# Kernel tuning notes

Measured on AMD Instinct MI355X. Metric: run time of the kernel, lower is better.

## Reference

```python
import jax, jax.numpy as jnp
import numpy as np

N_VOX = 500000
P, S, K = 2048, 64, 8          # pixels(rays), samples per ray, voxel neighbors per sample
F_M, F_H = 64, 128             # voxel feature dim, mlp hidden dim
FREQ_PE = 4
DEPTH_MIN, DEPTH_MAX = 1.0, 80.0
RAY_SAMPLE_STEPS = 64.0
EPS = 1e-10
IN_FEAT = F_M + 3 * FREQ_PE * 2  # 88


def lrelu(x):
    return jnp.where(x >= 0, x, 0.1 * x)  # LeakyReLU(0.1)


def posenc(x, L=FREQ_PE):
    # NeRF positional encoding: sin/cos(2^i * x), i in [0, L)
    freqs = 2.0 ** jnp.arange(L, dtype=x.dtype)          # [L]
    ang = x[..., None] * freqs                            # [..., 3, L]
    enc = jnp.concatenate([jnp.sin(ang), jnp.cos(ang)], axis=-1)  # [..., 3, 2L]
    return enc.reshape(x.shape[:-1] + (x.shape[-1] * 2 * L,))


def setup_inputs() -> dict:
    key = jax.random.key(0)
    ks = jax.random.split(key, 16)

    def xavier(k, fan_in, fan_out):
        return jax.random.normal(k, (fan_in, fan_out), jnp.float32) / np.sqrt(fan_in)

    inp = {
        'map_xyz': jax.random.normal(ks[0], (N_VOX, 3), jnp.float32),
        'map_feat': jax.random.normal(ks[1], (N_VOX, F_M), jnp.float32) * 0.05,
        'ind_voxel': jax.random.randint(ks[2], (P, S, K), 0, N_VOX),
        'sample_xyz': jax.random.normal(ks[3], (P, S, 3), jnp.float32),
        'dist_to_cam': jax.random.uniform(ks[4], (P, S), jnp.float32) * RAY_SAMPLE_STEPS,
        'W0': xavier(ks[5], IN_FEAT, F_H), 'b0': jnp.full((F_H,), 0.01, jnp.float32),
        'W1': xavier(ks[6], F_H, F_H),     'b1': jnp.full((F_H,), 0.01, jnp.float32),
        'W2': xavier(ks[7], F_H, F_H),     'b2': jnp.full((F_H,), 0.01, jnp.float32),
        'Wa0': xavier(ks[8], F_H, F_H // 2), 'ba0': jnp.full((F_H // 2,), 0.01, jnp.float32),
        'Wa1': xavier(ks[9], F_H // 2, 1),   'ba1': jnp.full((1,), 0.01, jnp.float32),
        'Wr0': xavier(ks[10], F_H, F_H // 2), 'br0': jnp.full((F_H // 2,), 0.01, jnp.float32),
        'Wr1': xavier(ks[11], F_H // 2, 3),   'br1': jnp.full((3,), 0.01, jnp.float32),
    }
    return inp


def reference(map_xyz, map_feat, ind_voxel, sample_xyz, dist_to_cam,
              W0, b0, W1, b1, W2, b2, Wa0, ba0, Wa1, ba1, Wr0, br0, Wr1, br1):
    # ---- voxel -> sample messages (func_msg_voxel_to_sample) ----
    voxel_xyz = map_xyz[ind_voxel]                       # [P,S,K,3] gather
    feat = map_feat[ind_voxel]                           # [P,S,K,F_M] gather
    offset = sample_xyz[:, :, None, :] - voxel_xyz       # [P,S,K,3]
    h = jnp.concatenate([feat, posenc(offset)], axis=-1) # [P,S,K,88]
    h = lrelu(h @ W0 + b0)
    h = lrelu(h @ W1 + b1)
    h = lrelu(h @ W2 + b2)                               # [P,S,K,F_H]
    w = jnp.exp(-10.0 * jnp.linalg.norm(offset, axis=-1))  # [P,S,K]
    w = w / jnp.sum(w, axis=-1, keepdims=True)
    # ---- reduce over K neighbors (func_reduce_voxel_to_sample) ----
    feat_s = jnp.sum(h * w[..., None], axis=2)           # [P,S,F_H]
    a = lrelu(feat_s @ Wa0 + ba0)
    alpha = jax.nn.sigmoid(a @ Wa1 + ba1)                # [P,S,1]
    r = lrelu(feat_s @ Wr0 + br0)
    rgb = jax.nn.sigmoid(r @ Wr1 + br1)                  # [P,S,3]
    # ---- sample -> pixel volume rendering (func_reduce_sample_to_pixel) ----
    dist = DEPTH_MIN + DEPTH_MAX * dist_to_cam / RAY_SAMPLE_STEPS  # [P,S]
    ones = jnp.ones((P, 1, 1), alpha.dtype)
    trans = jnp.cumprod(jnp.concatenate([ones, 1.0 - alpha + EPS], axis=1), axis=1)[:, :-1, :]
    blend = alpha * trans                                # [P,S,1]
    pixel_rgb = jnp.sum(rgb * blend, axis=1)             # [P,3]
    pixel_d = jnp.sum(dist[..., None] * blend, axis=1)   # [P,1]
    acc = jnp.sum(blend, axis=1)                         # [P,1]
    return jnp.concatenate([pixel_rgb, pixel_d, acc], axis=-1)  # [P,5]
```

## Files before the change

kernel.cpp:

```cpp
#include <hip/hip_runtime.h>

typedef __bf16 bf16_t;
typedef __bf16 bf16x2 __attribute__((ext_vector_type(2)));
typedef __bf16 bf16x4 __attribute__((ext_vector_type(4)));
typedef __bf16 bf16x8 __attribute__((ext_vector_type(8)));
typedef float  f32x4  __attribute__((ext_vector_type(4)));

#define NPIX 2048
#define NS   64
#define NK   8
#define NSAMP (NPIX*NS)
#define NROWS (NSAMP*NK)
#define TROWS 64
#define NTILES (NROWS/TROWS)
#define GRID   512
#define NIT    16
#define XSTR 104
#define HSTR 136

#define PK_W0 0
#define PK_W1 1536
#define PK_W2 3584
#define PK_WA 5632
#define PK_WR 6656
#define PK_TOT 7680

#define WS_AR_BYTES 122880

__global__ void pack_weights(const float* __restrict__ W0, const float* __restrict__ W1,
                             const float* __restrict__ W2, const float* __restrict__ Wa0,
                             const float* __restrict__ Wr0, bf16_t* __restrict__ dst0) {
  int tid = blockIdx.x * blockDim.x + threadIdx.x;
  if (tid >= PK_TOT * 8) return;
  const float* src; bf16_t* dst; int e, KD, ND, KS;
  if (tid < 12288)      { src = W0;  dst = dst0;         e = tid;         KD = 88;  ND = 128; KS = 3; }
  else if (tid < 28672) { src = W1;  dst = dst0 + 12288; e = tid - 12288; KD = 128; ND = 128; KS = 4; }
  else if (tid < 45056) { src = W2;  dst = dst0 + 28672; e = tid - 28672; KD = 128; ND = 128; KS = 4; }
  else if (tid < 53248) { src = Wa0; dst = dst0 + 45056; e = tid - 45056; KD = 128; ND = 64;  KS = 4; }
  else                  { src = Wr0; dst = dst0 + 53248; e = tid - 53248; KD = 128; ND = 64;  KS = 4; }
  int j = e & 7, l = (e >> 3) & 63, f = e >> 9;
  int s = f % KS, t = f / KS;
  int row = s * 32 + (l >> 4) * 8 + j;
  int col = t * 16 + (l & 15);
  float v = (row < KD) ? src[row * ND + col] : 0.f;
  dst[e] = (bf16_t)v;
}

__device__ __forceinline__ float lrelu(float v) { return fmaxf(v, 0.1f * v); }
__device__ __forceinline__ float sigmoidf(float x) { return 1.f / (1.f + __expf(-x)); }

__global__ __launch_bounds__(512, 4)
void nerf_main(const float* __restrict__ map_xyz, const float* __restrict__ map_feat,
               const int* __restrict__ ind, const float* __restrict__ sample_xyz,
               const float* __restrict__ b0g, const float* __restrict__ b1g,
               const float* __restrict__ b2g, const float* __restrict__ ba0g,
               const float* __restrict__ wa1g, const float* __restrict__ ba1g,
               const float* __restrict__ br0g, const float* __restrict__ wr1g,
               const float* __restrict__ br1g, const bf16_t* __restrict__ wpack,
               float* __restrict__ ar_out)
{
  __shared__ __align__(16) bf16_t sH0[TROWS * HSTR];
  __shared__ __align__(16) bf16_t sH1[TROWS * HSTR];
  __shared__ __align__(16) bf16_t sX[TROWS * XSTR];
  __shared__ __align__(16) bf16_t sFS[16 * HSTR];
  __shared__ __align__(16) bf16_t sAR[16 * HSTR];
  __shared__ __align__(16) bf16_t sFB[2048];
  __shared__ __align__(16) float sWtA[TROWS], sWtB[TROWS];
  __shared__ float sWsA[8], sWsB[8];
  __shared__ __align__(16) float sB0[128], sB1[128], sB2[128], sBH[128], sFBv[4];

  const int tid = threadIdx.x;
  const int wid = tid >> 6, l = tid & 63;
  const int q = l >> 4, n = l & 15;
  const int sr = tid >> 3, sp = tid & 7;

  const bf16x8* pk = (const bf16x8*)wpack;
  bf16x8 w0f[3], w1f[4], w2f[4], hdf[4];
#pragma unroll
  for (int s = 0; s < 3; s++) w0f[s] = pk[PK_W0 + (wid * 3 + s) * 64 + l];
#pragma unroll
  for (int s = 0; s < 4; s++) w1f[s] = pk[PK_W1 + (wid * 4 + s) * 64 + l];
#pragma unroll
  for (int s = 0; s < 4; s++) w2f[s] = pk[PK_W2 + (wid * 4 + s) * 64 + l];
#pragma unroll
  for (int s = 0; s < 4; s++)
    hdf[s] = pk[(wid < 4 ? PK_WA : PK_WR) + ((wid & 3) * 4 + s) * 64 + l];

  auto COMMIT = [&](int tile, bf16_t* X, float* wtbuf) {
    const int m = tile * TROWS + sr;
    const int idx = ind[m];
    const float4* fp = (const float4*)(map_feat + (size_t)idx * 64 + sp * 8);
    float4 f0 = fp[0], f1 = fp[1];
    bf16x8 v;
    v[0] = (bf16_t)f0.x; v[1] = (bf16_t)f0.y; v[2] = (bf16_t)f0.z; v[3] = (bf16_t)f0.w;
    v[4] = (bf16_t)f1.x; v[5] = (bf16_t)f1.y; v[6] = (bf16_t)f1.z; v[7] = (bf16_t)f1.w;
    *(bf16x8*)(X + sr * XSTR + sp * 8) = v;
    const int g = m >> 3;
    if (sp < 6) {
      const int d = sp >> 1;
      float o = sample_xyz[g * 3 + d] - map_xyz[idx * 3 + d];
      float s1 = __sinf(o), c1 = __cosf(o);
      float s2 = 2.f * s1 * c1, c2 = 1.f - 2.f * s1 * s1;
      float s4 = 2.f * s2 * c2, c4 = 1.f - 2.f * s2 * s2;
      float s8 = 2.f * s4 * c4, c8 = 1.f - 2.f * s4 * s4;
      bf16x4 e;
      if (sp & 1) { e[0] = (bf16_t)c1; e[1] = (bf16_t)c2; e[2] = (bf16_t)c4; e[3] = (bf16_t)c8; }
      else        { e[0] = (bf16_t)s1; e[1] = (bf16_t)s2; e[2] = (bf16_t)s4; e[3] = (bf16_t)s8; }
      *(bf16x4*)(X + sr * XSTR + 64 + d * 8 + (sp & 1) * 4) = e;
    } else if (sp == 6) {
      bf16x8 z = {};
      *(bf16x8*)(X + sr * XSTR + 88) = z;
    } else {
      float ox = sample_xyz[g * 3 + 0] - map_xyz[idx * 3 + 0];
      float oy = sample_xyz[g * 3 + 1] - map_xyz[idx * 3 + 1];
      float oz = sample_xyz[g * 3 + 2] - map_xyz[idx * 3 + 2];
      wtbuf[sr] = __expf(-10.f * sqrtf(ox * ox + oy * oy + oz * oz));
    }
  };

  auto L0 = [&](const bf16_t* X, bf16_t* Hout) {
    f32x4 bi = *(const f32x4*)(sB0 + wid * 16 + q * 4);
    f32x4 acc[4] = {bi, bi, bi, bi};
    __builtin_amdgcn_s_setprio(1);
#pragma unroll
    for (int st = 0; st < 4; st++)
#pragma unroll
      for (int s = 0; s < 3; s++) {
        bf16x8 b = *(const bf16x8*)(X + (st * 16 + n) * XSTR + s * 32 + q * 8);
        acc[st] = __builtin_amdgcn_mfma_f32_16x16x32_bf16(w0f[s], b, acc[st], 0, 0, 0);
      }
    __builtin_amdgcn_s_setprio(0);
#pragma unroll
    for (int st = 0; st < 4; st++) {
      bf16x4 o;
      o[0] = (bf16_t)lrelu(acc[st][0]);
      o[1] = (bf16_t)lrelu(acc[st][1]);
      o[2] = (bf16_t)lrelu(acc[st][2]);
      o[3] = (bf16_t)lrelu(acc[st][3]);
      *(bf16x4*)(Hout + (st * 16 + n) * HSTR + wid * 16 + q * 4) = o;
    }
  };

  auto LAYER = [&](const bf16_t* Hin, bf16_t* Hout, const bf16x8* wf, const float* bg) {
    f32x4 bi = *(const f32x4*)(bg + wid * 16 + q * 4);
    f32x4 acc[4] = {bi, bi, bi, bi};
    __builtin_amdgcn_s_setprio(1);
#pragma unroll
    for (int st = 0; st < 4; st++)
#pragma unroll
      for (int s = 0; s < 4; s++) {
        bf16x8 b = *(const bf16x8*)(Hin + (st * 16 + n) * HSTR + s * 32 + q * 8);
        acc[st] = __builtin_amdgcn_mfma_f32_16x16x32_bf16(wf[s], b, acc[st], 0, 0, 0);
      }
    __builtin_amdgcn_s_setprio(0);
#pragma unroll
    for (int st = 0; st < 4; st++) {
      bf16x4 o;
      o[0] = (bf16_t)lrelu(acc[st][0]);
      o[1] = (bf16_t)lrelu(acc[st][1]);
      o[2] = (bf16_t)lrelu(acc[st][2]);
      o[3] = (bf16_t)lrelu(acc[st][3]);
      *(bf16x4*)(Hout + (st * 16 + n) * HSTR + wid * 16 + q * 4) = o;
    }
  };

  auto KRED = [&](const bf16_t* Hin, const float* wt, const float* ws, bf16_t* FS) {
    int g = tid >> 6;
    int c = (tid & 63) * 2;
    float a0 = 0.f, a1 = 0.f;
#pragma unroll
    for (int k = 0; k < 8; k++) {
      float wk = wt[g * 8 + k];
      unsigned u = *(const unsigned*)(Hin + (g * 8 + k) * HSTR + c);
      a0 += wk * __uint_as_float(u << 16);
      a1 += wk * __uint_as_float(u & 0xffff0000u);
    }
    float inv = 1.f / ws[g];
    bf16x2 fo;
    fo[0] = (bf16_t)(a0 * inv);
    fo[1] = (bf16_t)(a1 * inv);
    *(bf16x2*)(FS + g * HSTR + c) = fo;
  };

  auto HEADS = [&](const bf16_t* FS, bf16_t* AR) {
    f32x4 ha = *(const f32x4*)(sBH + wid * 16 + q * 4);
    __builtin_amdgcn_s_setprio(1);
#pragma unroll
    for (int s = 0; s < 4; s++) {
      bf16x8 b = *(const bf16x8*)(FS + n * HSTR + s * 32 + q * 8);
      ha = __builtin_amdgcn_mfma_f32_16x16x32_bf16(hdf[s], b, ha, 0, 0, 0);
    }
    __builtin_amdgcn_s_setprio(0);
    if (n < 8) {
      const int base = (wid < 4) ? 64 : 0;
      bf16x4 o;
      o[0] = (bf16_t)lrelu(ha[0]);
      o[1] = (bf16_t)lrelu(ha[1]);
      o[2] = (bf16_t)lrelu(ha[2]);
      o[3] = (bf16_t)lrelu(ha[3]);
      *(bf16x4*)(AR + n * HSTR + base + (wid & 3) * 16 + q * 4) = o;
    }
  };

  auto FINALS = [&](int tile) {
    if (wid == 0) {
      f32x4 c = *(const f32x4*)sFBv;
#pragma unroll
      for (int s = 0; s < 4; s++) {
        bf16x8 a = *(const bf16x8*)(sFB + (s * 64 + l) * 8);
        bf16x8 b = *(const bf16x8*)(sAR + n * HSTR + s * 32 + q * 8);
        c = __builtin_amdgcn_mfma_f32_16x16x32_bf16(a, b, c, 0, 0, 0);
      }
      if (q == 0 && n < 8) {
        float4 o;
        o.x = sigmoidf(c[0]);
        o.y = sigmoidf(c[1]);
        o.z = sigmoidf(c[2]);
        o.w = sigmoidf(c[3]);
        ((float4*)ar_out)[tile * 8 + n] = o;
      }
    }
  };

  for (int i = tid; i < 8 * HSTR; i += 512) {
    sFS[8 * HSTR + i] = (bf16_t)0.f;
    sAR[8 * HSTR + i] = (bf16_t)0.f;
  }
  {
    int e0 = tid * 4;
    int jb = e0 & 7, ll = (e0 >> 3) & 63, s = e0 >> 9;
    int m = ll & 15;
#pragma unroll
    for (int ii = 0; ii < 4; ii++) {
      int k = s * 32 + (ll >> 4) * 8 + jb + ii;
      float v = 0.f;
      if (k < 64)  { if (m < 3) v = wr1g[k * 3 + m]; }
      else         { if (m == 3) v = wa1g[k - 64]; }
      sFB[e0 + ii] = (bf16_t)v;
    }
  }
  if (tid < 128)      sB0[tid] = b0g[tid];
  else if (tid < 256) sB1[tid - 128] = b1g[tid - 128];
  else if (tid < 384) sB2[tid - 256] = b2g[tid - 256];
  else { int t = tid - 384; sBH[t] = (t < 64) ? ba0g[t] : br0g[t - 64]; }
  if (tid < 4) sFBv[tid] = (tid < 3) ? br1g[tid] : ba1g[0];
  __syncthreads();

  for (int it = 0; it <= NIT; ++it) {
    const bool a_on = (it < NIT);
    const bool b_on = (it > 0);
    const int tA  = (int)blockIdx.x + (2 * it) * GRID;
    const int tAp = (int)blockIdx.x + (2 * it - 2) * GRID;
    const int tB  = (int)blockIdx.x + (2 * it + 1) * GRID;
    const int tBp = (int)blockIdx.x + (2 * it - 1) * GRID;

    if (a_on) COMMIT(tA, sX, sWtA);
    if (b_on) LAYER(sH0, sH1, w2f, sB2);
    if (b_on) FINALS(tAp);
    __syncthreads();

    if (a_on) L0(sX, sH0);
    if (b_on) KRED(sH1, sWtB, sWsB, sFS);
    if (a_on && tid < 8) {
      float ss = 0.f;
#pragma unroll
      for (int k = 0; k < 8; k++) ss += sWtA[tid * 8 + k];
      sWsA[tid] = ss;
    }
    __syncthreads();

    if (a_on) LAYER(sH0, sH1, w1f, sB1);
    if (b_on) HEADS(sFS, sAR);
    __syncthreads();

    if (a_on) COMMIT(tB, sX, sWtB);
    if (a_on) LAYER(sH1, sH0, w2f, sB2);
    if (b_on) FINALS(tBp);
    __syncthreads();

    if (it == NIT) break;

    L0(sX, sH1);
    KRED(sH0, sWtA, sWsA, sFS);
    if (tid < 8) {
      float ss = 0.f;
#pragma unroll
      for (int k = 0; k < 8; k++) ss += sWtB[tid * 8 + k];
      sWsB[tid] = ss;
    }
    __syncthreads();

    LAYER(sH1, sH0, w1f, sB1);
    HEADS(sFS, sAR);
    __syncthreads();
  }
}

__global__ __launch_bounds__(512)
void render_kernel(const float* __restrict__ ar, const float* __restrict__ dcam,
                   float* __restrict__ out) {
  int ray = blockIdx.x * 8 + (threadIdx.x >> 6);
  int s = threadIdx.x & 63;
  float4 v = ((const float4*)ar)[ray * 64 + s];
  float alpha = v.w;
  float t = 1.f - alpha + 1e-10f;
  float p = t;
#pragma unroll
  for (int d = 1; d < 64; d <<= 1) {
    float o = __shfl_up(p, d);
    if (s >= d) p *= o;
  }
  float pm1 = __shfl_up(p, 1);
  float T = (s == 0) ? 1.f : pm1;
  float bl = alpha * T;
  float dist = 1.f + 1.25f * dcam[ray * 64 + s];
  float cr = v.x * bl, cg = v.y * bl, cb = v.z * bl, cd = dist * bl, ca = bl;
#pragma unroll
  for (int d = 32; d > 0; d >>= 1) {
    cr += __shfl_xor(cr, d);
    cg += __shfl_xor(cg, d);
    cb += __shfl_xor(cb, d);
    cd += __shfl_xor(cd, d);
    ca += __shfl_xor(ca, d);
  }
  if (s == 0) {
    out[ray * 5 + 0] = cr; out[ray * 5 + 1] = cg; out[ray * 5 + 2] = cb;
    out[ray * 5 + 3] = cd; out[ray * 5 + 4] = ca;
  }
}

extern "C" void kernel_launch(void* const* d_in, const int* in_sizes, int n_in,
                              void* d_out, int out_size, void* d_ws, size_t ws_size,
                              hipStream_t stream) {
  const float* map_xyz    = (const float*)d_in[0];
  const float* map_feat   = (const float*)d_in[1];
  const int*   ind        = (const int*)d_in[2];
  const float* sample_xyz = (const float*)d_in[3];
  const float* dist_cam   = (const float*)d_in[4];
  const float* W0  = (const float*)d_in[5];
  const float* b0  = (const float*)d_in[6];
  const float* W1  = (const float*)d_in[7];
  const float* b1  = (const float*)d_in[8];
  const float* W2  = (const float*)d_in[9];
  const float* b2  = (const float*)d_in[10];
  const float* Wa0 = (const float*)d_in[11];
  const float* ba0 = (const float*)d_in[12];
  const float* Wa1 = (const float*)d_in[13];
  const float* ba1 = (const float*)d_in[14];
  const float* Wr0 = (const float*)d_in[15];
  const float* br0 = (const float*)d_in[16];
  const float* Wr1 = (const float*)d_in[17];
  const float* br1 = (const float*)d_in[18];

  bf16_t* wpack = (bf16_t*)d_ws;
  float*  ar    = (float*)((char*)d_ws + WS_AR_BYTES);

  pack_weights<<<240, 256, 0, stream>>>(W0, W1, W2, Wa0, Wr0, wpack);
  nerf_main<<<GRID, 512, 0, stream>>>(map_xyz, map_feat, ind, sample_xyz,
                                      b0, b1, b2, ba0, Wa1, ba1, br0, Wr1, br1,
                                      wpack, ar);
  render_kernel<<<256, 512, 0, stream>>>(ar, dist_cam, (float*)d_out);
}
```

Baseline: 393.9 us.

## Tile MLP layers 2x2 per wave to halve LDS activation reads

Each wave now computes a 32-column by 32-row output block instead of 16 columns by 64 rows. Every loaded activation fragment is reused across two weight fragments, which halves the LDS reads per MFMA. Holding twice as many weight fragments in registers raises register pressure, so the launch bounds drop to 2 blocks per SM and the grid is halved while each block runs twice as many iterations. That costs occupancy, which matters because latency hiding for the gather stage depends on it.

```diff
diff --git a/kernel.cpp b/kernel.cpp
--- a/kernel.cpp
+++ b/kernel.cpp
@@ -13,8 +13,8 @@
 #define NROWS (NSAMP*NK)
 #define TROWS 64
 #define NTILES (NROWS/TROWS)
-#define GRID   512
-#define NIT    16
+#define GRID   256
+#define NIT    32
 #define XSTR 104
 #define HSTR 136
 
@@ -49,7 +49,7 @@
 __device__ __forceinline__ float lrelu(float v) { return fmaxf(v, 0.1f * v); }
 __device__ __forceinline__ float sigmoidf(float x) { return 1.f / (1.f + __expf(-x)); }
 
-__global__ __launch_bounds__(512, 4)
+__global__ __launch_bounds__(512, 2)
 void nerf_main(const float* __restrict__ map_xyz, const float* __restrict__ map_feat,
                const int* __restrict__ ind, const float* __restrict__ sample_xyz,
                const float* __restrict__ b0g, const float* __restrict__ b1g,
@@ -72,16 +72,20 @@
   const int tid = threadIdx.x;
   const int wid = tid >> 6, l = tid & 63;
   const int q = l >> 4, n = l & 15;
+  const int wc = wid & 3, ws = wid >> 2;
   const int sr = tid >> 3, sp = tid & 7;
 
   const bf16x8* pk = (const bf16x8*)wpack;
-  bf16x8 w0f[3], w1f[4], w2f[4], hdf[4];
-#pragma unroll
-  for (int s = 0; s < 3; s++) w0f[s] = pk[PK_W0 + (wid * 3 + s) * 64 + l];
-#pragma unroll
-  for (int s = 0; s < 4; s++) w1f[s] = pk[PK_W1 + (wid * 4 + s) * 64 + l];
-#pragma unroll
-  for (int s = 0; s < 4; s++) w2f[s] = pk[PK_W2 + (wid * 4 + s) * 64 + l];
+  bf16x8 w0f[6], w1f[8], w2f[8], hdf[4];
+#pragma unroll
+  for (int m = 0; m < 2; m++) {
+#pragma unroll
+    for (int s = 0; s < 3; s++) w0f[m * 3 + s] = pk[PK_W0 + ((2 * wc + m) * 3 + s) * 64 + l];
+#pragma unroll
+    for (int s = 0; s < 4; s++) w1f[m * 4 + s] = pk[PK_W1 + ((2 * wc + m) * 4 + s) * 64 + l];
+#pragma unroll
+    for (int s = 0; s < 4; s++) w2f[m * 4 + s] = pk[PK_W2 + ((2 * wc + m) * 4 + s) * 64 + l];
+  }
 #pragma unroll
   for (int s = 0; s < 4; s++)
     hdf[s] = pk[(wid < 4 ? PK_WA : PK_WR) + ((wid & 3) * 4 + s) * 64 + l];
@@ -119,52 +123,74 @@
   };
 
   auto L0 = [&](const bf16_t* X, bf16_t* Hout) {
-    f32x4 bi = *(const f32x4*)(sB0 + wid * 16 + q * 4);
-    f32x4 acc[4] = {bi, bi, bi, bi};
+    f32x4 acc[2][2];
+#pragma unroll
+    for (int m = 0; m < 2; m++) {
+      f32x4 bi = *(const f32x4*)(sB0 + wc * 32 + m * 16 + q * 4);
+      acc[m][0] = bi; acc[m][1] = bi;
+    }
     __builtin_amdgcn_s_setprio(1);
 #pragma unroll
-    for (int st = 0; st < 4; st++)
-#pragma unroll
-      for (int s = 0; s < 3; s++) {
-        bf16x8 b = *(const bf16x8*)(X + (st * 16 + n) * XSTR + s * 32 + q * 8);
-        acc[st] = __builtin_amdgcn_mfma_f32_16x16x32_bf16(w0f[s], b, acc[st], 0, 0, 0);
+    for (int st = 0; st < 2; st++) {
+      bf16x8 b[3];
+#pragma unroll
+      for (int s = 0; s < 3; s++)
+        b[s] = *(const bf16x8*)(X + (ws * 32 + st * 16 + n) * XSTR + s * 32 + q * 8);
+#pragma unroll
+      for (int m = 0; m < 2; m++)
+#pragma unroll
+        for (int s = 0; s < 3; s++)
+          acc[m][st] = __builtin_amdgcn_mfma_f32_16x16x32_bf16(w0f[m * 3 + s], b[s], acc[m][st], 0, 0, 0);
+    }
+    __builtin_amdgcn_s_setprio(0);
+#pragma unroll
+    for (int m = 0; m < 2; m++)
+#pragma unroll
+      for (int st = 0; st < 2; st++) {
+        bf16x4 o;
+        o[0] = (bf16_t)lrelu(acc[m][st][0]);
+        o[1] = (bf16_t)lrelu(acc[m][st][1]);
+        o[2] = (bf16_t)lrelu(acc[m][st][2]);
+        o[3] = (bf16_t)lrelu(acc[m][st][3]);
+        *(bf16x4*)(Hout + (ws * 32 + st * 16 + n) * HSTR + wc * 32 + m * 16 + q * 4) = o;
       }
+  };
+
+  auto LAYER = [&](const bf16_t* Hin, bf16_t* Hout, const bf16x8* wf, const float* bg) {
+    f32x4 acc[2][2];
+#pragma unroll
+    for (int m = 0; m < 2; m++) {
+      f32x4 bi = *(const f32x4*)(bg + wc * 32 + m * 16 + q * 4);
+      acc[m][0] = bi; acc[m][1] = bi;
+    }
+    __builtin_amdgcn_s_setprio(1);
+#pragma unroll
+    for (int st = 0; st < 2; st++) {
+      bf16x8 b[4];
+#pragma unroll
+      for (int s = 0; s < 4; s++)
+        b[s] = *(const bf16x8*)(Hin + (ws * 32 + st * 16 + n) * HSTR + s * 32 + q * 8);
+#pragma unroll
+      for (int m = 0; m < 2; m++)
+#pragma unroll
+        for (int s = 0; s < 4; s++)
+          acc[m][st] = __builtin_amdgcn_mfma_f32_16x16x32_bf16(wf[m * 4 + s], b[s], acc[m][st], 0, 0, 0);
+    }
     __builtin_amdgcn_s_setprio(0);
 #pragma unroll
-    for (int st = 0; st < 4; st++) {
-      bf16x4 o;
-      o[0] = (bf16_t)lrelu(acc[st][0]);
-      o[1] = (bf16_t)lrelu(acc[st][1]);
-      o[2] = (bf16_t)lrelu(acc[st][2]);
-      o[3] = (bf16_t)lrelu(acc[st][3]);
-      *(bf16x4*)(Hout + (st * 16 + n) * HSTR + wid * 16 + q * 4) = o;
-    }
-  };
-
-  auto LAYER = [&](const bf16_t* Hin, bf16_t* Hout, const bf16x8* wf, const float* bg) {
-    f32x4 bi = *(const f32x4*)(bg + wid * 16 + q * 4);
-    f32x4 acc[4] = {bi, bi, bi, bi};
-    __builtin_amdgcn_s_setprio(1);
-#pragma unroll
-    for (int st = 0; st < 4; st++)
-#pragma unroll
-      for (int s = 0; s < 4; s++) {
-        bf16x8 b = *(const bf16x8*)(Hin + (st * 16 + n) * HSTR + s * 32 + q * 8);
-        acc[st] = __builtin_amdgcn_mfma_f32_16x16x32_bf16(wf[s], b, acc[st], 0, 0, 0);
+    for (int m = 0; m < 2; m++)
+#pragma unroll
+      for (int st = 0; st < 2; st++) {
+        bf16x4 o;
+        o[0] = (bf16_t)lrelu(acc[m][st][0]);
+        o[1] = (bf16_t)lrelu(acc[m][st][1]);
+        o[2] = (bf16_t)lrelu(acc[m][st][2]);
+        o[3] = (bf16_t)lrelu(acc[m][st][3]);
+        *(bf16x4*)(Hout + (ws * 32 + st * 16 + n) * HSTR + wc * 32 + m * 16 + q * 4) = o;
       }
-    __builtin_amdgcn_s_setprio(0);
-#pragma unroll
-    for (int st = 0; st < 4; st++) {
-      bf16x4 o;
-      o[0] = (bf16_t)lrelu(acc[st][0]);
-      o[1] = (bf16_t)lrelu(acc[st][1]);
-      o[2] = (bf16_t)lrelu(acc[st][2]);
-      o[3] = (bf16_t)lrelu(acc[st][3]);
-      *(bf16x4*)(Hout + (st * 16 + n) * HSTR + wid * 16 + q * 4) = o;
-    }
-  };
-
-  auto KRED = [&](const bf16_t* Hin, const float* wt, const float* ws, bf16_t* FS) {
+  };
+
+  auto KRED = [&](const bf16_t* Hin, const float* wt, const float* ws_, bf16_t* FS) {
     int g = tid >> 6;
     int c = (tid & 63) * 2;
     float a0 = 0.f, a1 = 0.f;
@@ -175,7 +201,7 @@
       a0 += wk * __uint_as_float(u << 16);
       a1 += wk * __uint_as_float(u & 0xffff0000u);
     }
-    float inv = 1.f / ws[g];
+    float inv = 1.f / ws_[g];
     bf16x2 fo;
     fo[0] = (bf16_t)(a0 * inv);
     fo[1] = (bf16_t)(a1 * inv);
```

Measured after the change: 426.8 us. 8.3% more time.

## Fuse volume rendering into main kernel via contiguous per-block tile assignment

Applied to the files above, without the earlier changes.

Tiles are reassigned so each block processes contiguous tiles covering four whole rays, which lets per-sample rgb/alpha accumulate in shared memory. Wave 0 then runs the transmittance scan and compositing directly, removing the separate render kernel and the global round trip for the intermediate buffer. Address arithmetic in the MFMA loops is also hoisted into base pointers. The cost is that wave 0 now does extra serial shuffle work inside the pipelined loop, and the contiguous tile mapping changes the global memory access pattern.

```diff
diff --git a/kernel.cpp b/kernel.cpp
--- a/kernel.cpp
+++ b/kernel.cpp
@@ -24,8 +24,6 @@
 #define PK_WA 5632
 #define PK_WR 6656
 #define PK_TOT 7680
-
-#define WS_AR_BYTES 122880
 
 __global__ void pack_weights(const float* __restrict__ W0, const float* __restrict__ W1,
                              const float* __restrict__ W2, const float* __restrict__ Wa0,
@@ -52,12 +50,13 @@
 __global__ __launch_bounds__(512, 4)
 void nerf_main(const float* __restrict__ map_xyz, const float* __restrict__ map_feat,
                const int* __restrict__ ind, const float* __restrict__ sample_xyz,
+               const float* __restrict__ dcam,
                const float* __restrict__ b0g, const float* __restrict__ b1g,
                const float* __restrict__ b2g, const float* __restrict__ ba0g,
                const float* __restrict__ wa1g, const float* __restrict__ ba1g,
                const float* __restrict__ br0g, const float* __restrict__ wr1g,
                const float* __restrict__ br1g, const bf16_t* __restrict__ wpack,
-               float* __restrict__ ar_out)
+               float* __restrict__ out)
 {
   __shared__ __align__(16) bf16_t sH0[TROWS * HSTR];
   __shared__ __align__(16) bf16_t sH1[TROWS * HSTR];
@@ -65,6 +64,7 @@
   __shared__ __align__(16) bf16_t sFS[16 * HSTR];
   __shared__ __align__(16) bf16_t sAR[16 * HSTR];
   __shared__ __align__(16) bf16_t sFB[2048];
+  __shared__ __align__(16) float4 sPix[2 * 64];
   __shared__ __align__(16) float sWtA[TROWS], sWtB[TROWS];
   __shared__ float sWsA[8], sWsB[8];
   __shared__ __align__(16) float sB0[128], sB1[128], sB2[128], sBH[128], sFBv[4];
@@ -121,12 +121,14 @@
   auto L0 = [&](const bf16_t* X, bf16_t* Hout) {
     f32x4 bi = *(const f32x4*)(sB0 + wid * 16 + q * 4);
     f32x4 acc[4] = {bi, bi, bi, bi};
+    const bf16_t* rb = X + n * XSTR + q * 8;
+    bf16_t* wb = Hout + n * HSTR + wid * 16 + q * 4;
     __builtin_amdgcn_s_setprio(1);
 #pragma unroll
     for (int st = 0; st < 4; st++)
 #pragma unroll
       for (int s = 0; s < 3; s++) {
-        bf16x8 b = *(const bf16x8*)(X + (st * 16 + n) * XSTR + s * 32 + q * 8);
+        bf16x8 b = *(const bf16x8*)(rb + st * 16 * XSTR + s * 32);
         acc[st] = __builtin_amdgcn_mfma_f32_16x16x32_bf16(w0f[s], b, acc[st], 0, 0, 0);
       }
     __builtin_amdgcn_s_setprio(0);
@@ -137,19 +139,21 @@
       o[1] = (bf16_t)lrelu(acc[st][1]);
       o[2] = (bf16_t)lrelu(acc[st][2]);
       o[3] = (bf16_t)lrelu(acc[st][3]);
-      *(bf16x4*)(Hout + (st * 16 + n) * HSTR + wid * 16 + q * 4) = o;
+      *(bf16x4*)(wb + st * 16 * HSTR) = o;
     }
   };
 
   auto LAYER = [&](const bf16_t* Hin, bf16_t* Hout, const bf16x8* wf, const float* bg) {
     f32x4 bi = *(const f32x4*)(bg + wid * 16 + q * 4);
     f32x4 acc[4] = {bi, bi, bi, bi};
+    const bf16_t* rb = Hin + n * HSTR + q * 8;
+    bf16_t* wb = Hout + n * HSTR + wid * 16 + q * 4;
     __builtin_amdgcn_s_setprio(1);
 #pragma unroll
     for (int st = 0; st < 4; st++)
 #pragma unroll
       for (int s = 0; s < 4; s++) {
-        bf16x8 b = *(const bf16x8*)(Hin + (st * 16 + n) * HSTR + s * 32 + q * 8);
+        bf16x8 b = *(const bf16x8*)(rb + st * 16 * HSTR + s * 32);
         acc[st] = __builtin_amdgcn_mfma_f32_16x16x32_bf16(wf[s], b, acc[st], 0, 0, 0);
       }
     __builtin_amdgcn_s_setprio(0);
@@ -160,22 +164,23 @@
       o[1] = (bf16_t)lrelu(acc[st][1]);
       o[2] = (bf16_t)lrelu(acc[st][2]);
       o[3] = (bf16_t)lrelu(acc[st][3]);
-      *(bf16x4*)(Hout + (st * 16 + n) * HSTR + wid * 16 + q * 4) = o;
-    }
-  };
-
-  auto KRED = [&](const bf16_t* Hin, const float* wt, const float* ws, bf16_t* FS) {
+      *(bf16x4*)(wb + st * 16 * HSTR) = o;
+    }
+  };
+
+  auto KRED = [&](const bf16_t* Hin, const float* wt, const float* ws_, bf16_t* FS) {
     int g = tid >> 6;
     int c = (tid & 63) * 2;
+    const bf16_t* kb = Hin + g * 8 * HSTR + c;
     float a0 = 0.f, a1 = 0.f;
 #pragma unroll
     for (int k = 0; k < 8; k++) {
       float wk = wt[g * 8 + k];
-      unsigned u = *(const unsigned*)(Hin + (g * 8 + k) * HSTR + c);
+      unsigned u = *(const unsigned*)(kb + k * HSTR);
       a0 += wk * __uint_as_float(u << 16);
       a1 += wk * __uint_as_float(u & 0xffff0000u);
     }
-    float inv = 1.f / ws[g];
+    float inv = 1.f / ws_[g];
     bf16x2 fo;
     fo[0] = (bf16_t)(a0 * inv);
     fo[1] = (bf16_t)(a1 * inv);
@@ -184,10 +189,11 @@
 
   auto HEADS = [&](const bf16_t* FS, bf16_t* AR) {
     f32x4 ha = *(const f32x4*)(sBH + wid * 16 + q * 4);
+    const bf16_t* rb = FS + n * HSTR + q * 8;
     __builtin_amdgcn_s_setprio(1);
 #pragma unroll
     for (int s = 0; s < 4; s++) {
-      bf16x8 b = *(const bf16x8*)(FS + n * HSTR + s * 32 + q * 8);
+      bf16x8 b = *(const bf16x8*)(rb + s * 32);
       ha = __builtin_amdgcn_mfma_f32_16x16x32_bf16(hdf[s], b, ha, 0, 0, 0);
     }
     __builtin_amdgcn_s_setprio(0);
@@ -202,22 +208,53 @@
     }
   };
 
-  auto FINALS = [&](int tile) {
+  auto FINALS = [&](int k, int st, int pix) {
     if (wid == 0) {
       f32x4 c = *(const f32x4*)sFBv;
+      const bf16_t* ab = sFB + l * 8;
+      const bf16_t* rb = sAR + n * HSTR + q * 8;
 #pragma unroll
       for (int s = 0; s < 4; s++) {
-        bf16x8 a = *(const bf16x8*)(sFB + (s * 64 + l) * 8);
-        bf16x8 b = *(const bf16x8*)(sAR + n * HSTR + s * 32 + q * 8);
+        bf16x8 a = *(const bf16x8*)(ab + s * 512);
+        bf16x8 b = *(const bf16x8*)(rb + s * 32);
         c = __builtin_amdgcn_mfma_f32_16x16x32_bf16(a, b, c, 0, 0, 0);
       }
+      float4* px = (float4*)sPix + st * 64;
       if (q == 0 && n < 8) {
         float4 o;
         o.x = sigmoidf(c[0]);
         o.y = sigmoidf(c[1]);
         o.z = sigmoidf(c[2]);
         o.w = sigmoidf(c[3]);
-        ((float4*)ar_out)[tile * 8 + n] = o;
+        px[(k & 7) * 8 + n] = o;
+      }
+      if ((k & 7) == 7) {
+        float4 v = px[l];
+        float dc = dcam[pix * 64 + l];
+        float alpha = v.w;
+        float p = 1.f - alpha + 1e-10f;
+#pragma unroll
+        for (int d = 1; d < 64; d <<= 1) {
+          float o2 = __shfl_up(p, d);
+          if (l >= d) p *= o2;
+        }
+        float pm1 = __shfl_up(p, 1);
+        float T = (l == 0) ? 1.f : pm1;
+        float bl = alpha * T;
+        float dist = 1.f + 1.25f * dc;
+        float cr = v.x * bl, cg = v.y * bl, cb = v.z * bl, cd = dist * bl, ca = bl;
+#pragma unroll
+        for (int d = 32; d > 0; d >>= 1) {
+          cr += __shfl_xor(cr, d);
+          cg += __shfl_xor(cg, d);
+          cb += __shfl_xor(cb, d);
+          cd += __shfl_xor(cd, d);
+          ca += __shfl_xor(ca, d);
+        }
+        if (l == 0) {
+          out[pix * 5 + 0] = cr; out[pix * 5 + 1] = cg; out[pix * 5 + 2] = cb;
+          out[pix * 5 + 3] = cd; out[pix * 5 + 4] = ca;
+        }
       }
     }
   };
@@ -246,17 +283,19 @@
   if (tid < 4) sFBv[tid] = (tid < 3) ? br1g[tid] : ba1g[0];
   __syncthreads();
 
+  const int base = (int)blockIdx.x * 32;
+  const int bP = (int)blockIdx.x * 4;
+
   for (int it = 0; it <= NIT; ++it) {
     const bool a_on = (it < NIT);
     const bool b_on = (it > 0);
-    const int tA  = (int)blockIdx.x + (2 * it) * GRID;
-    const int tAp = (int)blockIdx.x + (2 * it - 2) * GRID;
-    const int tB  = (int)blockIdx.x + (2 * it + 1) * GRID;
-    const int tBp = (int)blockIdx.x + (2 * it - 1) * GRID;
+    const int tA = base + it;
+    const int tB = base + 16 + it;
+    const int kp = it - 1;
 
     if (a_on) COMMIT(tA, sX, sWtA);
     if (b_on) LAYER(sH0, sH1, w2f, sB2);
-    if (b_on) FINALS(tAp);
+    if (b_on) FINALS(kp, 0, bP + (kp >> 3));
     __syncthreads();
 
     if (a_on) L0(sX, sH0);
@@ -275,7 +314,7 @@
 
     if (a_on) COMMIT(tB, sX, sWtB);
     if (a_on) LAYER(sH1, sH0, w2f, sB2);
-    if (b_on) FINALS(tBp);
+    if (b_on) FINALS(kp, 1, bP + 2 + (kp >> 3));
     __syncthreads();
 
     if (it == NIT) break;
@@ -293,39 +332,6 @@
     LAYER(sH1, sH0, w1f, sB1);
     HEADS(sFS, sAR);
     __syncthreads();
-  }
-}
-
-__global__ __launch_bounds__(512)
-void render_kernel(const float* __restrict__ ar, const float* __restrict__ dcam,
-                   float* __restrict__ out) {
-  int ray = blockIdx.x * 8 + (threadIdx.x >> 6);
-  int s = threadIdx.x & 63;
-  float4 v = ((const float4*)ar)[ray * 64 + s];
-  float alpha = v.w;
-  float t = 1.f - alpha + 1e-10f;
-  float p = t;
-#pragma unroll
-  for (int d = 1; d < 64; d <<= 1) {
-    float o = __shfl_up(p, d);
-    if (s >= d) p *= o;
-  }
-  float pm1 = __shfl_up(p, 1);
-  float T = (s == 0) ? 1.f : pm1;
-  float bl = alpha * T;
-  float dist = 1.f + 1.25f * dcam[ray * 64 + s];
-  float cr = v.x * bl, cg = v.y * bl, cb = v.z * bl, cd = dist * bl, ca = bl;
-#pragma unroll
-  for (int d = 32; d > 0; d >>= 1) {
-    cr += __shfl_xor(cr, d);
-    cg += __shfl_xor(cg, d);
-    cb += __shfl_xor(cb, d);
-    cd += __shfl_xor(cd, d);
-    ca += __shfl_xor(ca, d);
-  }
-  if (s == 0) {
-    out[ray * 5 + 0] = cr; out[ray * 5 + 1] = cg; out[ray * 5 + 2] = cb;
-    out[ray * 5 + 3] = cd; out[ray * 5 + 4] = ca;
   }
 }
 
@@ -353,11 +359,9 @@
   const float* br1 = (const float*)d_in[18];
 
   bf16_t* wpack = (bf16_t*)d_ws;
-  float*  ar    = (float*)((char*)d_ws + WS_AR_BYTES);
 
   pack_weights<<<240, 256, 0, stream>>>(W0, W1, W2, Wa0, Wr0, wpack);
-  nerf_main<<<GRID, 512, 0, stream>>>(map_xyz, map_feat, ind, sample_xyz,
+  nerf_main<<<GRID, 512, 0, stream>>>(map_xyz, map_feat, ind, sample_xyz, dist_cam,
                                       b0, b1, b2, ba0, Wa1, ba1, br0, Wr1, br1,
-                                      wpack, ar);
-  render_kernel<<<256, 512, 0, stream>>>(ar, dist_cam, (float*)d_out);
+                                      wpack, (float*)d_out);
 }
```

Measured after the change: 398.9 us. No clear change (+1.2%).
